# Kernel tuning notes

Measured on AMD Instinct MI355X. Metric: run time of the kernel, lower is better.

The kernel has to match this reference:

```python
import jax, jax.numpy as jnp
import numpy as np

KEEP_RATIO = 0.7  # fully-annealed keep ratio (epoch >= 2*warmup_epochs)


def setup_inputs() -> dict:
    key = jax.random.key(0)
    k0, k1, k2 = jax.random.split(key, 3)
    B, H, W, C, HID = 16, 128, 128, 256, 128
    N = H * W
    tokens = jax.random.normal(k0, (B, N, C), dtype=jnp.float32)
    # xavier_uniform-ish init for the scorer MLP
    lim1 = float(np.sqrt(6.0 / (C + HID)))
    lim2 = float(np.sqrt(6.0 / (HID + 1)))
    w1 = jax.random.uniform(k1, (C, HID), minval=-lim1, maxval=lim1, dtype=jnp.float32)
    b1 = jnp.zeros((HID,), dtype=jnp.float32)
    w2 = jax.random.uniform(k2, (HID, 1), minval=-lim2, maxval=lim2, dtype=jnp.float32)
    b2 = jnp.zeros((1,), dtype=jnp.float32)
    return {"tokens": tokens, "w1": w1, "b1": b1, "w2": w2, "b2": b2}


def reference(tokens, w1, b1, w2, b2):
    # tokens: [B, N, C]; importance scorer: fc1 -> GELU(exact) -> fc2 -> squeeze
    B, N, C = tokens.shape
    num_keep = int(N * KEEP_RATIO)  # static; min_tokens=10 << num_keep
    h = jax.nn.gelu(jnp.einsum("bnc,ch->bnh", tokens, w1) + b1, approximate=False)
    scores = (jnp.einsum("bnh,ho->bno", h, w2) + b2)[..., 0]  # [B, N]
    # top-k token selection, then sort kept indices to preserve spatial order
    _, top_idx = jax.lax.top_k(scores, num_keep)          # [B, K]
    kept_indices = jnp.sort(top_idx, axis=-1)              # [B, K]
    pruned_tokens = jnp.take_along_axis(tokens, kept_indices[..., None], axis=1)  # [B, K, C]
    return pruned_tokens, kept_indices, scores
```

## Files before the change

### kernel.cpp

```cpp
#include <hip/hip_runtime.h>
#include <math.h>

#define B_ 16
#define N_ 16384
#define C_ 256
#define H_ 128
#define K_ 11468
#define G_ ((B_ * N_) / 16)

typedef __attribute__((ext_vector_type(8))) short s16x8;
typedef __attribute__((ext_vector_type(4))) float f32x4;
typedef __attribute__((ext_vector_type(4))) unsigned int u32x4;

__device__ __forceinline__ unsigned short f2bf(float f) {
  unsigned u = __builtin_bit_cast(unsigned, f);
  return (unsigned short)((u + 0x7FFFu + ((u >> 16) & 1u)) >> 16);
}
__device__ __forceinline__ unsigned fkey(float f) {
  unsigned u = __builtin_bit_cast(unsigned, f);
  return (u & 0x80000000u) ? ~u : (u | 0x80000000u);
}

__device__ __forceinline__ float gelu_fast(float h) {
  const float t = 0.5f * h * h;
  const float u = 0.147f * t;
  const float num = t * (1.2732395f + u);
  const float den = 1.0f + u;
  const float r = num * __builtin_amdgcn_rcpf(den);
  const float e = __builtin_amdgcn_exp2f(r * -1.44269504f);
  const float s = __builtin_amdgcn_sqrtf(fmaxf(1.0f - e, 0.0f));
  const unsigned sgn = __builtin_bit_cast(unsigned, h) & 0x80000000u;
  const float erfv = __builtin_bit_cast(float, __builtin_bit_cast(unsigned, s) | sgn);
  return 0.5f * h * (1.0f + erfv);
}

__global__ void k_prep(const float* __restrict__ w1, unsigned short* __restrict__ w1sw) {
  int i = blockIdx.x * blockDim.x + threadIdx.x;
  if (i < C_ * H_) {
    int c = i / H_, r = i % H_;
    int c16 = c >> 3, j = c & 7;
    w1sw[r * 256 + ((c16 ^ (r & 31)) << 3) + j] = f2bf(w1[i]);
  }
}

__global__ __launch_bounds__(256) void k_score(
    const float* __restrict__ tokens, const unsigned short* __restrict__ w1sw,
    const float* __restrict__ b1, const float* __restrict__ w2,
    const float* __restrict__ b2, float* __restrict__ scores_out) {
  __shared__ unsigned short lds[H_ * C_];

  {
    const f32x4* src = reinterpret_cast<const f32x4*>(w1sw);
    f32x4* dst = reinterpret_cast<f32x4*>(lds);
    const int t = threadIdx.x;
#pragma unroll
    for (int i = 0; i < 16; ++i) dst[t + i * 256] = src[t + i * 256];
  }
  __syncthreads();

  const int lane = threadIdx.x & 63;
  const int l15 = lane & 15;
  const int l4 = lane >> 4;
  const int wid = (blockIdx.x * blockDim.x + threadIdx.x) >> 6;
  const int nw = (gridDim.x * blockDim.x) >> 6;

  float b1v[8], w2v[8];
#pragma unroll
  for (int nb = 0; nb < 8; ++nb) {
    b1v[nb] = b1[nb * 16 + l15];
    w2v[nb] = w2[nb * 16 + l15];
  }
  const float b2v = b2[0];

  for (int g = wid; g < G_; g += nw) {
    const float* tp = tokens + (size_t)(g * 16 + l15) * C_ + l4 * 8;

    f32x4 v[16];
#pragma unroll
    for (int kk = 0; kk < 8; ++kk) {
      v[2 * kk] = *reinterpret_cast<const f32x4*>(tp + kk * 32);
      v[2 * kk + 1] = *reinterpret_cast<const f32x4*>(tp + kk * 32 + 4);
    }
    u32x4 a[8];
#pragma unroll
    for (int kk = 0; kk < 8; ++kk) {
      a[kk][0] = __builtin_amdgcn_perm(__builtin_bit_cast(unsigned, v[2 * kk][1]),
                                       __builtin_bit_cast(unsigned, v[2 * kk][0]), 0x07060302u);
      a[kk][1] = __builtin_amdgcn_perm(__builtin_bit_cast(unsigned, v[2 * kk][3]),
                                       __builtin_bit_cast(unsigned, v[2 * kk][2]), 0x07060302u);
      a[kk][2] = __builtin_amdgcn_perm(__builtin_bit_cast(unsigned, v[2 * kk + 1][1]),
                                       __builtin_bit_cast(unsigned, v[2 * kk + 1][0]), 0x07060302u);
      a[kk][3] = __builtin_amdgcn_perm(__builtin_bit_cast(unsigned, v[2 * kk + 1][3]),
                                       __builtin_bit_cast(unsigned, v[2 * kk + 1][2]), 0x07060302u);
    }

    float p[4] = {0.f, 0.f, 0.f, 0.f};
#pragma unroll
    for (int nb = 0; nb < 8; ++nb) {
      f32x4 acc = (f32x4){0.f, 0.f, 0.f, 0.f};
#pragma unroll
      for (int kk = 0; kk < 8; ++kk) {
        const int e0 = (((l4 + kk * 4) ^ l15) << 3);
        const int off = (nb & 1) ? (e0 ^ 128) : e0;
        s16x8 bf = *reinterpret_cast<const s16x8*>(lds + nb * 4096 + l15 * 256 + off);
        acc = __builtin_amdgcn_mfma_f32_16x16x32_bf16(
            __builtin_bit_cast(s16x8, a[kk]), bf, acc, 0, 0, 0);
      }
#pragma unroll
      for (int r = 0; r < 4; ++r) p[r] += gelu_fast(acc[r] + b1v[nb]) * w2v[nb];
    }

#pragma unroll
    for (int r = 0; r < 4; ++r) {
      float s = p[r];
      s += __shfl_xor(s, 1);
      s += __shfl_xor(s, 2);
      s += __shfl_xor(s, 4);
      s += __shfl_xor(s, 8);
      p[r] = s + b2v;
    }
    if (l15 == 0) {
      const int rb = g * 16 + l4 * 4;
#pragma unroll
      for (int r = 0; r < 4; ++r) scores_out[rb + r] = p[r];
    }
  }
}

__device__ unsigned block_exscan_1024(unsigned v, volatile unsigned* wsum) {
  const int lane = threadIdx.x & 63;
  const int w = threadIdx.x >> 6;
  unsigned x = v;
#pragma unroll
  for (int d = 1; d < 64; d <<= 1) {
    unsigned t = __shfl_up(x, d);
    if (lane >= d) x += t;
  }
  if (lane == 63) wsum[w] = x;
  __syncthreads();
  if (threadIdx.x == 0) {
    unsigned s = 0;
    for (int i = 0; i < 16; ++i) {
      unsigned t = wsum[i];
      wsum[i] = s;
      s += t;
    }
  }
  __syncthreads();
  unsigned r = wsum[w] + x - v;
  __syncthreads();
  return r;
}

__global__ __launch_bounds__(1024) void k_select(const float* __restrict__ scores_f,
                                                 int* __restrict__ kept,
                                                 float* __restrict__ out_idx) {
  __shared__ unsigned hist[256];
  __shared__ unsigned wsum[16];
  __shared__ unsigned sh_prefix, sh_rk;
  const int b = blockIdx.x;
  const int tid = threadIdx.x;
  const float* sp = scores_f + (size_t)b * N_;

  unsigned prefix = 0;
  unsigned rk = K_;
  for (int pass = 0; pass < 4; ++pass) {
    const int shift = 24 - pass * 8;
    if (tid < 256) hist[tid] = 0;
    __syncthreads();
    const unsigned pmask = pass ? (0xFFFFFFFFu << (shift + 8)) : 0u;
    for (int i = tid; i < N_; i += 1024) {
      unsigned k = fkey(sp[i]);
      if ((k & pmask) == prefix) atomicAdd(&hist[(k >> shift) & 255u], 1u);
    }
    __syncthreads();
    unsigned h = (tid < 256) ? hist[255 - tid] : 0u;
    unsigned s = block_exscan_1024(h, wsum);
    if (tid < 256 && s < rk && s + h >= rk) {
      sh_prefix = prefix | ((unsigned)(255 - tid) << shift);
      sh_rk = rk - s;
    }
    __syncthreads();
    prefix = sh_prefix;
    rk = sh_rk;
    __syncthreads();
  }
  const unsigned Tkey = prefix;
  const unsigned need = rk;

  const int i0 = tid * 16;
  unsigned neq = 0;
  for (int j = 0; j < 16; ++j) {
    unsigned k = fkey(sp[i0 + j]);
    neq += (k == Tkey);
  }
  unsigned eq_base = block_exscan_1024(neq, wsum);

  unsigned kcnt = 0;
  {
    unsigned eqr = eq_base;
    for (int j = 0; j < 16; ++j) {
      unsigned k = fkey(sp[i0 + j]);
      bool kp = (k > Tkey) || ((k == Tkey) && (eqr < need));
      eqr += (k == Tkey);
      kcnt += kp;
    }
  }
  unsigned pos = block_exscan_1024(kcnt, wsum);
  {
    unsigned eqr = eq_base;
    for (int j = 0; j < 16; ++j) {
      unsigned k = fkey(sp[i0 + j]);
      bool kp = (k > Tkey) || ((k == Tkey) && (eqr < need));
      eqr += (k == Tkey);
      if (kp) {
        kept[(size_t)b * K_ + pos] = i0 + j;
        out_idx[(size_t)b * K_ + pos] = (float)(i0 + j);
        ++pos;
      }
    }
  }
}

__global__ __launch_bounds__(256) void k_gather(const float* __restrict__ tokens,
                                                const int* __restrict__ kept,
                                                float* __restrict__ outp) {
  const int wid = (blockIdx.x * blockDim.x + threadIdx.x) >> 6;
  const int lane = threadIdx.x & 63;
  if (wid >= B_ * K_) return;
  const int b = wid / K_;
  const int idx = kept[wid];
  const f32x4 v = *reinterpret_cast<const f32x4*>(tokens + ((size_t)b * N_ + idx) * C_ + lane * 4);
  *reinterpret_cast<f32x4*>(outp + (size_t)wid * C_ + lane * 4) = v;
}

extern "C" void kernel_launch(void* const* d_in, const int* in_sizes, int n_in,
                              void* d_out, int out_size, void* d_ws, size_t ws_size,
                              hipStream_t stream) {
  const float* tokens = (const float*)d_in[0];
  const float* w1 = (const float*)d_in[1];
  const float* b1 = (const float*)d_in[2];
  const float* w2 = (const float*)d_in[3];
  const float* b2 = (const float*)d_in[4];

  float* out = (float*)d_out;
  float* out_pruned = out;
  float* out_idx = out + (size_t)B_ * K_ * C_;
  float* out_scores = out_idx + (size_t)B_ * K_;

  char* ws = (char*)d_ws;
  unsigned short* w1sw = (unsigned short*)ws;
  int* kept = (int*)(ws + 0x10000);

  k_prep<<<dim3((C_ * H_ + 255) / 256), dim3(256), 0, stream>>>(w1, w1sw);
  k_score<<<dim3(1024), dim3(256), 0, stream>>>(tokens, w1sw, b1, w2, b2, out_scores);
  k_select<<<dim3(B_), dim3(1024), 0, stream>>>(out_scores, kept, out_idx);
  k_gather<<<dim3((B_ * K_ + 3) / 4), dim3(256), 0, stream>>>(tokens, kept, out_pruned);
}
```

Measured before the change: 195.1 us.

## Keep W1 in registers, stage token tiles through double-buffered LDS

The scoring kernel used to copy all of W1 (64KB) into LDS and have each wave stream its own 16-token group. Now each wave keeps a 32-column slice of W1 resident in registers. Token tiles are converted to bf16 and staged in a small double-buffered LDS area shared by all four waves, with a cross-wave reduction of partial scores through LDS. The goal is to drop the large LDS footprint, which limited occupancy, and the repeated B-operand LDS reads. In exchange it adds two block barriers per tile and a 1024-block grid of 16 tiles each.

```diff
diff --git a/kernel.cpp b/kernel.cpp
--- a/kernel.cpp
+++ b/kernel.cpp
@@ -7,6 +7,8 @@
 #define H_ 128
 #define K_ 11468
 #define G_ ((B_ * N_) / 16)
+#define GPB_ 16
+#define NBLK_ (G_ / GPB_)
 
 typedef __attribute__((ext_vector_type(8))) short s16x8;
 typedef __attribute__((ext_vector_type(4))) float f32x4;
@@ -19,6 +21,10 @@
 __device__ __forceinline__ unsigned fkey(float f) {
   unsigned u = __builtin_bit_cast(unsigned, f);
   return (u & 0x80000000u) ? ~u : (u | 0x80000000u);
+}
+__device__ __forceinline__ unsigned pk2(float hi, float lo) {
+  return __builtin_amdgcn_perm(__builtin_bit_cast(unsigned, hi),
+                               __builtin_bit_cast(unsigned, lo), 0x07060302u);
 }
 
 __device__ __forceinline__ float gelu_fast(float h) {
@@ -34,96 +40,115 @@
   return 0.5f * h * (1.0f + erfv);
 }
 
-__global__ void k_prep(const float* __restrict__ w1, unsigned short* __restrict__ w1sw) {
+__global__ void k_prep(const float* __restrict__ w1, unsigned short* __restrict__ w1t) {
   int i = blockIdx.x * blockDim.x + threadIdx.x;
   if (i < C_ * H_) {
-    int c = i / H_, r = i % H_;
-    int c16 = c >> 3, j = c & 7;
-    w1sw[r * 256 + ((c16 ^ (r & 31)) << 3) + j] = f2bf(w1[i]);
+    int c = i / H_, h = i % H_;
+    w1t[h * C_ + c] = f2bf(w1[i]);
   }
 }
 
 __global__ __launch_bounds__(256) void k_score(
-    const float* __restrict__ tokens, const unsigned short* __restrict__ w1sw,
+    const float* __restrict__ tokens, const unsigned short* __restrict__ w1t,
     const float* __restrict__ b1, const float* __restrict__ w2,
     const float* __restrict__ b2, float* __restrict__ scores_out) {
-  __shared__ unsigned short lds[H_ * C_];
-
-  {
-    const f32x4* src = reinterpret_cast<const f32x4*>(w1sw);
-    f32x4* dst = reinterpret_cast<f32x4*>(lds);
-    const int t = threadIdx.x;
-#pragma unroll
-    for (int i = 0; i < 16; ++i) dst[t + i * 256] = src[t + i * 256];
-  }
-  __syncthreads();
-
-  const int lane = threadIdx.x & 63;
+  __shared__ unsigned short lds_a[2][8 * 64 * 8];
+  __shared__ float lds_c[4][16];
+
+  const int tid = threadIdx.x;
+  const int lane = tid & 63;
   const int l15 = lane & 15;
   const int l4 = lane >> 4;
-  const int wid = (blockIdx.x * blockDim.x + threadIdx.x) >> 6;
-  const int nw = (gridDim.x * blockDim.x) >> 6;
-
-  float b1v[8], w2v[8];
-#pragma unroll
-  for (int nb = 0; nb < 8; ++nb) {
-    b1v[nb] = b1[nb * 16 + l15];
-    w2v[nb] = w2[nb * 16 + l15];
-  }
+  const int w = tid >> 6;
+
+  s16x8 bfr0[8], bfr1[8];
+  const int row0 = (2 * w) * 16 + l15;
+  const int row1 = row0 + 16;
+#pragma unroll
+  for (int kk = 0; kk < 8; ++kk) {
+    bfr0[kk] = *reinterpret_cast<const s16x8*>(w1t + row0 * 256 + (l4 + 4 * kk) * 8);
+    bfr1[kk] = *reinterpret_cast<const s16x8*>(w1t + row1 * 256 + (l4 + 4 * kk) * 8);
+  }
+  const float b1v0 = b1[row0], b1v1 = b1[row1];
+  const float w2v0 = w2[row0], w2v1 = w2[row1];
   const float b2v = b2[0];
 
-  for (int g = wid; g < G_; g += nw) {
-    const float* tp = tokens + (size_t)(g * 16 + l15) * C_ + l4 * 8;
-
-    f32x4 v[16];
+  const int sr = tid >> 4;
+  const int sq = tid & 15;
+
+  const int g0 = blockIdx.x * GPB_;
+  f32x4 vv[4];
+
+  {
+    const float* p = tokens + ((size_t)(g0 * 16 + sr)) * 256 + sq * 16;
+#pragma unroll
+    for (int i2 = 0; i2 < 4; ++i2) vv[i2] = *reinterpret_cast<const f32x4*>(p + 4 * i2);
+#pragma unroll
+    for (int j = 0; j < 2; ++j) {
+      u32x4 o;
+      o[0] = pk2(vv[2 * j][1], vv[2 * j][0]);
+      o[1] = pk2(vv[2 * j][3], vv[2 * j][2]);
+      o[2] = pk2(vv[2 * j + 1][1], vv[2 * j + 1][0]);
+      o[3] = pk2(vv[2 * j + 1][3], vv[2 * j + 1][2]);
+      const int c = 2 * sq + j;
+      *reinterpret_cast<u32x4*>(&lds_a[0][((c >> 2) * 64 + (c & 3) * 16 + sr) * 8]) = o;
+    }
+  }
+  __syncthreads();
+
+  int cur = 0;
+  for (int i = 0; i < GPB_; ++i) {
+    const int g = g0 + i;
+    if (i + 1 < GPB_) {
+      const float* p = tokens + ((size_t)((g + 1) * 16 + sr)) * 256 + sq * 16;
+#pragma unroll
+      for (int i2 = 0; i2 < 4; ++i2) vv[i2] = *reinterpret_cast<const f32x4*>(p + 4 * i2);
+    }
+
+    f32x4 acc0 = (f32x4){0.f, 0.f, 0.f, 0.f};
+    f32x4 acc1 = (f32x4){0.f, 0.f, 0.f, 0.f};
 #pragma unroll
     for (int kk = 0; kk < 8; ++kk) {
-      v[2 * kk] = *reinterpret_cast<const f32x4*>(tp + kk * 32);
-      v[2 * kk + 1] = *reinterpret_cast<const f32x4*>(tp + kk * 32 + 4);
-    }
-    u32x4 a[8];
-#pragma unroll
-    for (int kk = 0; kk < 8; ++kk) {
-      a[kk][0] = __builtin_amdgcn_perm(__builtin_bit_cast(unsigned, v[2 * kk][1]),
-                                       __builtin_bit_cast(unsigned, v[2 * kk][0]), 0x07060302u);
-      a[kk][1] = __builtin_amdgcn_perm(__builtin_bit_cast(unsigned, v[2 * kk][3]),
-                                       __builtin_bit_cast(unsigned, v[2 * kk][2]), 0x07060302u);
-      a[kk][2] = __builtin_amdgcn_perm(__builtin_bit_cast(unsigned, v[2 * kk + 1][1]),
-                                       __builtin_bit_cast(unsigned, v[2 * kk + 1][0]), 0x07060302u);
-      a[kk][3] = __builtin_amdgcn_perm(__builtin_bit_cast(unsigned, v[2 * kk + 1][3]),
-                                       __builtin_bit_cast(unsigned, v[2 * kk + 1][2]), 0x07060302u);
-    }
-
-    float p[4] = {0.f, 0.f, 0.f, 0.f};
-#pragma unroll
-    for (int nb = 0; nb < 8; ++nb) {
-      f32x4 acc = (f32x4){0.f, 0.f, 0.f, 0.f};
-#pragma unroll
-      for (int kk = 0; kk < 8; ++kk) {
-        const int e0 = (((l4 + kk * 4) ^ l15) << 3);
-        const int off = (nb & 1) ? (e0 ^ 128) : e0;
-        s16x8 bf = *reinterpret_cast<const s16x8*>(lds + nb * 4096 + l15 * 256 + off);
-        acc = __builtin_amdgcn_mfma_f32_16x16x32_bf16(
-            __builtin_bit_cast(s16x8, a[kk]), bf, acc, 0, 0, 0);
-      }
-#pragma unroll
-      for (int r = 0; r < 4; ++r) p[r] += gelu_fast(acc[r] + b1v[nb]) * w2v[nb];
-    }
-
-#pragma unroll
-    for (int r = 0; r < 4; ++r) {
-      float s = p[r];
+      s16x8 a = *reinterpret_cast<const s16x8*>(&lds_a[cur][(kk * 64 + lane) * 8]);
+      acc0 = __builtin_amdgcn_mfma_f32_16x16x32_bf16(a, bfr0[kk], acc0, 0, 0, 0);
+      acc1 = __builtin_amdgcn_mfma_f32_16x16x32_bf16(a, bfr1[kk], acc1, 0, 0, 0);
+    }
+
+    float p4[4];
+#pragma unroll
+    for (int rr = 0; rr < 4; ++rr) {
+      float s = gelu_fast(acc0[rr] + b1v0) * w2v0 + gelu_fast(acc1[rr] + b1v1) * w2v1;
       s += __shfl_xor(s, 1);
       s += __shfl_xor(s, 2);
       s += __shfl_xor(s, 4);
       s += __shfl_xor(s, 8);
-      p[r] = s + b2v;
+      p4[rr] = s;
     }
     if (l15 == 0) {
-      const int rb = g * 16 + l4 * 4;
-#pragma unroll
-      for (int r = 0; r < 4; ++r) scores_out[rb + r] = p[r];
-    }
+#pragma unroll
+      for (int rr = 0; rr < 4; ++rr) lds_c[w][l4 * 4 + rr] = p4[rr];
+    }
+    __syncthreads();
+
+    if (tid < 16) {
+      scores_out[g * 16 + tid] =
+          lds_c[0][tid] + lds_c[1][tid] + lds_c[2][tid] + lds_c[3][tid] + b2v;
+    }
+    if (i + 1 < GPB_) {
+#pragma unroll
+      for (int j = 0; j < 2; ++j) {
+        u32x4 o;
+        o[0] = pk2(vv[2 * j][1], vv[2 * j][0]);
+        o[1] = pk2(vv[2 * j][3], vv[2 * j][2]);
+        o[2] = pk2(vv[2 * j + 1][1], vv[2 * j + 1][0]);
+        o[3] = pk2(vv[2 * j + 1][3], vv[2 * j + 1][2]);
+        const int c = 2 * sq + j;
+        *reinterpret_cast<u32x4*>(
+            &lds_a[cur ^ 1][((c >> 2) * 64 + (c & 3) * 16 + sr) * 8]) = o;
+      }
+    }
+    __syncthreads();
+    cur ^= 1;
   }
 }
 
@@ -249,11 +274,11 @@
   float* out_scores = out_idx + (size_t)B_ * K_;
 
   char* ws = (char*)d_ws;
-  unsigned short* w1sw = (unsigned short*)ws;
+  unsigned short* w1t = (unsigned short*)ws;
   int* kept = (int*)(ws + 0x10000);
 
-  k_prep<<<dim3((C_ * H_ + 255) / 256), dim3(256), 0, stream>>>(w1, w1sw);
-  k_score<<<dim3(1024), dim3(256), 0, stream>>>(tokens, w1sw, b1, w2, b2, out_scores);
+  k_prep<<<dim3((C_ * H_ + 255) / 256), dim3(256), 0, stream>>>(w1, w1t);
+  k_score<<<dim3(NBLK_), dim3(256), 0, stream>>>(tokens, w1t, b1, w2, b2, out_scores);
   k_select<<<dim3(B_), dim3(1024), 0, stream>>>(out_scores, kept, out_idx);
   k_gather<<<dim3((B_ * K_ + 3) / 4), dim3(256), 0, stream>>>(tokens, kept, out_pruned);
 }
```

New measurement: 168.3 us. 13.8% less time.
